# Performance work log

Measured on AMD Instinct MI355X. Metric: run time of the kernel, lower is better.

The kernel has to match this reference:

```python
import jax
import jax.numpy as jnp
import numpy as np

KSIZE, STRIDE, RATE, FUSE_K, SCALE = 3, 1, 2, 3, 10.0
ESCAPE_NAN = 1e-4


def _same_pad(x, k, s):
    # replicates torch same_padding: asymmetric zero pad so out = ceil(H/s)
    H, W = x.shape[2], x.shape[3]
    oh, ow = -(-H // s), -(-W // s)
    ph = max(0, (oh - 1) * s + k - H)
    pw = max(0, (ow - 1) * s + k - W)
    return jnp.pad(x, ((0, 0), (0, 0), (ph // 2, ph - ph // 2), (pw // 2, pw - pw // 2)))


def _extract_patches(x, k, s):
    # torch extract_image_patches: -> [B, L, C, k, k] with L = out_h*out_w
    x = _same_pad(x, k, s)
    B, C, H, W = x.shape
    Ho, Wo = (H - k) // s + 1, (W - k) // s + 1
    slices = [x[:, :, i:i + Ho * s:s, j:j + Wo * s:s] for i in range(k) for j in range(k)]
    p = jnp.stack(slices, axis=2).reshape(B, C, k, k, Ho, Wo)
    return p.transpose(0, 4, 5, 1, 2, 3).reshape(B, Ho * Wo, C, k, k)


def _contextual_attention(f, b, mask):
    dn = ('NCHW', 'OIHW', 'NCHW')
    # raw background patches for the final deconv: k = 2*rate, stride = rate
    raw_pat = _extract_patches(b, 2 * RATE, RATE * STRIDE)  # [B, L, C, 4, 4]
    # nearest-neighbor 1/rate downsample (torch F.interpolate nearest, sf=0.5)
    f_ds = f[:, :, ::RATE, ::RATE]
    b_ds = b[:, :, ::RATE, ::RATE]
    m_ds = mask[:, :, ::RATE, ::RATE]
    B, C, Hf, Wf = f_ds.shape
    Hb, Wb = b_ds.shape[2], b_ds.shape[3]
    b_pat = _extract_patches(b_ds, KSIZE, STRIDE)  # [B, L, C, 3, 3], L = Hb*Wb
    m_pat = _extract_patches(m_ds, KSIZE, STRIDE)[0]  # [L, 1, 3, 3] (first sample only, as in torch)
    mm = (jnp.mean(m_pat, axis=(1, 2, 3)) == 0.0).astype(f.dtype)[None, :, None, None]  # [1, L, 1, 1]
    fuse_w = jnp.eye(FUSE_K, dtype=f.dtype).reshape(1, 1, FUSE_K, FUSE_K)

    def per_item(xi, wi, raw_wi):
        # xi: [C,Hf,Wf]; wi: [L,C,3,3]; raw_wi: [L,C,4,4]
        max_wi = jnp.sqrt(jnp.sum(wi * wi + ESCAPE_NAN, axis=(1, 2, 3), keepdims=True))
        wi_n = wi / max_wi
        # matching conv: scores [1, L, Hf, Wf]
        yi = jax.lax.conv_general_dilated(xi[None], wi_n, (1, 1), ((1, 1), (1, 1)), dimension_numbers=dn)
        # fuse: identity-diagonal 3x3 conv along (bg_idx, fg_idx) twice with transposes
        yi = yi.reshape(1, 1, Hb * Wb, Hf * Wf)
        yi = jax.lax.conv_general_dilated(yi, fuse_w, (1, 1), ((1, 1), (1, 1)), dimension_numbers=dn)
        yi = yi.reshape(Hb, Wb, Hf, Wf).transpose(1, 0, 3, 2).reshape(1, 1, Hb * Wb, Hf * Wf)
        yi = jax.lax.conv_general_dilated(yi, fuse_w, (1, 1), ((1, 1), (1, 1)), dimension_numbers=dn)
        yi = yi.reshape(Wb, Hb, Wf, Hf).transpose(1, 0, 3, 2).reshape(1, Hb * Wb, Hf, Wf)
        yi = yi * mm
        yi = jax.nn.softmax(yi * SCALE, axis=1) * mm
        # conv_transpose2d(yi, raw_wi[I=L,O=C], stride=rate, padding=1) / 4
        w2 = jnp.flip(raw_wi, (2, 3)).transpose(1, 0, 2, 3)  # [C, L, 4, 4]
        pad = 2 * RATE - 1 - 1  # k - 1 - torch_padding = 2
        out = jax.lax.conv_general_dilated(yi, w2, (1, 1), ((pad, pad), (pad, pad)),
                                           lhs_dilation=(RATE, RATE), dimension_numbers=dn) / 4.0
        return out[0]

    return jax.vmap(per_item)(f_ds, b_pat, raw_pat)  # [B, C, H, W]


def setup_inputs() -> dict:
    key = jax.random.key(0)
    k1, k2 = jax.random.split(key)
    B, C, H, W = 2, 128, 128, 128
    f = jax.random.normal(k1, (B, C, H, W), dtype=jnp.float32)
    b = jax.random.normal(k2, (B, C, H, W), dtype=jnp.float32)
    mask = jnp.zeros((B, 1, H, W), dtype=jnp.float32)
    return {"f": f, "b": b, "mask": mask}


def reference(f, b, mask):
    return _contextual_attention(f, b, mask)
```

## Files before the change

### kernel.cpp

```cpp
#include <hip/hip_runtime.h>
#include <math.h>

#define CDIM 128
#define HF   128
#define WF   128
#define NP   4096
#define NCHUNK 64

typedef __attribute__((ext_vector_type(8))) short short8;
typedef __attribute__((ext_vector_type(16))) float f16a;
typedef float __attribute__((ext_vector_type(4), aligned(16))) f4a16;
typedef float __attribute__((ext_vector_type(4), aligned(4)))  f4u;

__device__ inline ushort f2bf(float x) {
  union { float f; unsigned u; } v; v.f = x;
  unsigned r = v.u + 0x7fff + ((v.u >> 16) & 1);
  return (ushort)(r >> 16);
}
__device__ inline float bf2f(ushort h) {
  union { unsigned u; float f; } v; v.u = ((unsigned)h) << 16; return v.f;
}

__device__ inline void gl2lds16(const ushort* g, ushort* l) {
  __builtin_amdgcn_global_load_lds((const __attribute__((address_space(1))) void*)g,
                                   (__attribute__((address_space(3))) void*)l, 16, 0, 0);
}

__global__ __launch_bounds__(256) void k_prep(const float* __restrict__ f,
                                              const float* __restrict__ b,
                                              ushort* __restrict__ fcat,
                                              ushort* __restrict__ bcat,
                                              float* __restrict__ s2) {
  int idx = blockIdx.x * 256 + threadIdx.x;
  int c = idx & 127, pos = idx >> 7;
  int x = pos & 63, y = pos >> 6;
  int src = c * 16384 + y * 256 + x * 2;
  float fv = f[src], bv = b[src];
  ushort fh = f2bf(fv); ushort fl = f2bf(fv - bf2f(fh));
  ushort bh = f2bf(bv); ushort bl = f2bf(bv - bf2f(bh));
  size_t base = (size_t)pos * 384;
  fcat[base + c] = fh; fcat[base + 128 + c] = fl; fcat[base + 256 + c] = fh;
  bcat[base + c] = bh; bcat[base + 128 + c] = bh; bcat[base + 256 + c] = bl;
  float sq = bv * bv;
#pragma unroll
  for (int off = 32; off; off >>= 1) sq += __shfl_down(sq, off);
  __shared__ float wsum[4];
  if ((threadIdx.x & 63) == 0) wsum[threadIdx.x >> 6] = sq;
  __syncthreads();
  if (threadIdx.x == 0) s2[blockIdx.x * 2]     = wsum[0] + wsum[1];
  if (threadIdx.x == 1) s2[blockIdx.x * 2 + 1] = wsum[2] + wsum[3];
}

__global__ __launch_bounds__(256) void k_mmpnorm(const float* __restrict__ mask,
                                                 const float* __restrict__ s2,
                                                 float* __restrict__ mmp,
                                                 float* __restrict__ rnrm) {
  int bx = blockIdx.x, t = threadIdx.x;
  if (bx < 16) {
    int a = bx * 256 + t;
    int yb = a & 63, xb = a >> 6;
    float s = 0.f;
    for (int dy = -1; dy <= 1; ++dy)
      for (int dx = -1; dx <= 1; ++dx) {
        int y = yb + dy, x = xb + dx;
        if ((unsigned)y < 64u && (unsigned)x < 64u)
          s += mask[y * 256 + x * 2];
      }
    mmp[a] = (s == 0.0f) ? 1.0f : 0.0f;
  } else {
    int p = (bx - 16) * 256 + t;
    int xb = p & 63, yb = p >> 6;
    float s = 0.f;
    for (int dy = -1; dy <= 1; ++dy)
      for (int dx = -1; dx <= 1; ++dx) {
        int y = yb + dy, x = xb + dx;
        if ((unsigned)y < 64u && (unsigned)x < 64u) s += s2[y * 64 + x];
      }
    rnrm[p] = rsqrtf(s + 1152.0f * 1.0e-4f);
  }
}

__global__ __launch_bounds__(512) void k_mfma_gemm(const ushort* __restrict__ A,
                                                   const ushort* __restrict__ B,
                                                   float* __restrict__ Out,
                                                   int Kdim, int lda, int ldb, int ldo,
                                                   long osplit) {
  __shared__ ushort As[2][256 * 64];
  __shared__ ushort Bs[2][256 * 64];
  const int tid = threadIdx.x;
  const int wave = tid >> 6, lane = tid & 63;
  const int l32 = lane & 31, khalf = lane >> 5;
  const int m0 = blockIdx.y * 256, n0 = blockIdx.x * 256;
  const int wm = (wave >> 2) * 128, wn = (wave & 3) * 64;
  const int srow = lane >> 3;
  const int gperm = ((lane & 7) ^ srow) * 8;

  const int koff = blockIdx.z * Kdim;
  A += koff; B += koff;
  Out += (size_t)blockIdx.z * osplit;

  const ushort* Ag = A + (size_t)(m0 + wave * 8 + srow) * lda + gperm;
  const ushort* Bg = B + (size_t)(n0 + wave * 8 + srow) * ldb + gperm;
  ushort* AsW = &As[0][0] + (wave * 8) * 64;
  ushort* BsW = &Bs[0][0] + (wave * 8) * 64;

#define STG_A(sl, tt, q) gl2lds16(Ag + (size_t)((q) * 64) * lda + ((tt) << 6), \
                                  AsW + (sl) * 16384 + (q) * 4096)
#define STG_B(sl, tt, q) gl2lds16(Bg + (size_t)((q) * 64) * ldb + ((tt) << 6), \
                                  BsW + (sl) * 16384 + (q) * 4096)

  f16a acc[4][2];
#pragma unroll
  for (int u = 0; u < 4; ++u)
#pragma unroll
    for (int v = 0; v < 2; ++v)
#pragma unroll
      for (int r = 0; r < 16; ++r) acc[u][v][r] = 0.f;

  const int NT = Kdim >> 6;

#pragma unroll
  for (int q = 0; q < 4; ++q) { STG_A(0, 0, q); STG_B(0, 0, q); }
  asm volatile("s_waitcnt vmcnt(0)" ::: "memory");
  __builtin_amdgcn_s_barrier();
  __builtin_amdgcn_sched_barrier(0);

  for (int t = 0; t < NT; ++t) {
    const int sl = t & 1;
    const ushort* Ar = &As[sl][0];
    const ushort* Br = &Bs[sl][0];
    short8 af[2][4], bf[2][2];

#define FRAG_READS(sidx) do { \
  _Pragma("unroll") for (int u = 0; u < 4; ++u) { \
    int am = wm + u * 32 + l32; \
    int ga = (((sidx) * 2 + khalf) ^ (am & 7)) * 8; \
    af[(sidx) & 1][u] = *reinterpret_cast<const short8*>(&Ar[am * 64 + ga]); } \
  _Pragma("unroll") for (int v = 0; v < 2; ++v) { \
    int bn = wn + v * 32 + l32; \
    int gb = (((sidx) * 2 + khalf) ^ (bn & 7)) * 8; \
    bf[(sidx) & 1][v] = *reinterpret_cast<const short8*>(&Br[bn * 64 + gb]); } \
} while (0)

    FRAG_READS(0);
    if (t + 1 < NT) {
#pragma unroll
      for (int q = 0; q < 4; ++q) STG_A(sl ^ 1, t + 1, q);
    }
    FRAG_READS(1);
    if (t + 1 < NT) {
#pragma unroll
      for (int q = 0; q < 4; ++q) STG_B(sl ^ 1, t + 1, q);
    }
#pragma unroll
    for (int s = 0; s < 4; ++s) {
      if (s == 1) FRAG_READS(2);
      if (s == 2) FRAG_READS(3);
      __builtin_amdgcn_s_setprio(1);
#pragma unroll
      for (int u = 0; u < 4; ++u)
#pragma unroll
        for (int v = 0; v < 2; ++v)
          acc[u][v] = __builtin_amdgcn_mfma_f32_32x32x16_bf16(af[s & 1][u], bf[s & 1][v],
                                                              acc[u][v], 0, 0, 0);
      __builtin_amdgcn_s_setprio(0);
    }
    if (t + 1 < NT) {
      asm volatile("s_waitcnt vmcnt(0)" ::: "memory");
      __builtin_amdgcn_s_barrier();
      __builtin_amdgcn_sched_barrier(0);
    }
#undef FRAG_READS
  }

#pragma unroll
  for (int u = 0; u < 4; ++u)
#pragma unroll
    for (int v = 0; v < 2; ++v)
#pragma unroll
      for (int r = 0; r < 16; ++r) {
        int row = (r & 3) + 8 * (r >> 2) + 4 * khalf;
        Out[(size_t)(m0 + wm + u * 32 + row) * ldo + (n0 + wn + v * 32 + l32)] = acc[u][v][r];
      }
#undef STG_A
#undef STG_B
}

__global__ __launch_bounds__(256) void k_s0(const float* __restrict__ D,
                                            const float* __restrict__ rnrm,
                                            float* __restrict__ S0) {
  int p = ((blockIdx.x & 7) << 9) | (blockIdx.x >> 3);
  int yb = p >> 6, xb = p & 63;
  float rp = rnrm[p];
  int t = threadIdx.x;
#pragma unroll
  for (int it = 0; it < 4; ++it) {
    int q = (it * 256 + t) << 2;
    int qy = q >> 6, qx = q & 63;
    f4a16 acc = (f4a16){0.f, 0.f, 0.f, 0.f};
#pragma unroll
    for (int dy = -1; dy <= 1; ++dy) {
      if ((unsigned)(yb + dy) >= 64u) continue;
      if ((unsigned)(qy + dy) >= 64u) continue;
#pragma unroll
      for (int dx = -1; dx <= 1; ++dx) {
        if ((unsigned)(xb + dx) >= 64u) continue;
        int delta = dy * 64 + dx;
        const float* base = D + (size_t)(p + delta) * 4096;
        f4u v;
        if (dx == -1 && qx == 0) {
          f4u r = *(const f4u*)(base + q + delta + 1);
          v = (f4u){0.f, r.x, r.y, r.z};
        } else {
          v = *(const f4u*)(base + q + delta);
          if (dx == 1 && qx == 60) v.w = 0.f;
        }
        acc += v;
      }
    }
    acc *= rp;
    *(f4a16*)(S0 + ((size_t)p << 12) + q) = acc;
  }
}

__global__ __launch_bounds__(256) void k_fuse1(const float* __restrict__ S0,
                                               float* __restrict__ Yp) {
  __shared__ float row[4160];
  int i = ((blockIdx.x & 7) << 9) | (blockIdx.x >> 3);
  int t = threadIdx.x;
  const float* r0 = S0 + (size_t)(i - 1) * 4096;
  const float* r1 = S0 + (size_t)i * 4096;
  const float* r2 = S0 + (size_t)(i + 1) * 4096;
  bool up = (i > 0), dn = (i < 4095);
#pragma unroll
  for (int jj = 0; jj < 4; ++jj) {
    int j = (jj * 256 + t) << 2;
    f4u s = *(const f4u*)(r1 + j);
    if (up) {
      f4u a;
      if (j == 0) { f4u r = *(const f4u*)r0; a = (f4u){0.f, r.x, r.y, r.z}; }
      else a = *(const f4u*)(r0 + j - 1);
      s += a;
    }
    if (dn) {
      f4u d = *(const f4u*)(r2 + j + 1);
      if (j == 4092) d.w = 0.f;
      s += d;
    }
    int base = j + (j >> 6);
    row[base + 0] = s.x; row[base + 1] = s.y; row[base + 2] = s.z; row[base + 3] = s.w;
  }
  __syncthreads();
  int a = ((i & 63) << 6) | (i >> 6);
  float* orow = Yp + ((size_t)a << 12);
#pragma unroll
  for (int bb = 0; bb < 4; ++bb) {
    int b4 = (bb * 256 + t) << 2;
    f4a16 o;
#pragma unroll
    for (int k = 0; k < 4; ++k) {
      int jT = (((b4 + k) & 63) << 6) | ((b4 + k) >> 6);
      o[k] = row[jT + (jT >> 6)];
    }
    *(f4a16*)(orow + b4) = o;
  }
}

__global__ __launch_bounds__(256) void k_smax_part(const float* __restrict__ Yp,
                                                   const float* __restrict__ mmp,
                                                   float* __restrict__ pm,
                                                   float* __restrict__ ps) {
  int v = (blockIdx.x * 256 + threadIdx.x) << 2;
  int chunk = blockIdx.y;
  f4a16 m = (f4a16){-1e30f, -1e30f, -1e30f, -1e30f};
  f4a16 s = (f4a16){0.f, 0.f, 0.f, 0.f};
  int u0 = chunk * (4096 / NCHUNK);
  for (int u = u0; u < u0 + (4096 / NCHUNK); ++u) {
    const float* row = Yp + ((size_t)u << 12);
    f4u tv = *(const f4u*)(row + v);
    if (u > 0) {
      f4u a;
      if (v == 0) { f4u r = *(const f4u*)(row - 4096); a = (f4u){0.f, r.x, r.y, r.z}; }
      else a = *(const f4u*)(row - 4096 + v - 1);
      tv += a;
    }
    if (u < 4095) {
      f4u d = *(const f4u*)(row + 4096 + v + 1);
      if (v == 4092) d.w = 0.f;
      tv += d;
    }
    float g = 10.0f * mmp[u];
    f4u x = tv * g;
#pragma unroll
    for (int l = 0; l < 4; ++l) {
      float xl = x[l];
      if (xl > m[l]) { s[l] = s[l] * __expf(m[l] - xl) + 1.0f; m[l] = xl; }
      else           { s[l] += __expf(xl - m[l]); }
    }
  }
  *(f4a16*)(pm + chunk * NP + v) = m;
  *(f4a16*)(ps + chunk * NP + v) = s;
}

__global__ __launch_bounds__(256) void k_epilogue(const float* __restrict__ Yp,
                                                  const float* __restrict__ pm,
                                                  const float* __restrict__ ps,
                                                  const float* __restrict__ mmp,
                                                  ushort* __restrict__ AT,
                                                  const float* __restrict__ bimg,
                                                  ushort* __restrict__ VtT) {
  __shared__ float T[64][65];
  __shared__ float pmS[4][64];
  __shared__ float psS[4][64];
  __shared__ float mS[64];
  __shared__ float rsS[64];
  int gx = blockIdx.x;
  int t = threadIdx.x;
  if (gx < 4096) {
    int a0 = (gx & 63) * 64, b0 = (gx >> 6) * 64;
    int j = t & 63, grp = t >> 6;
    float m = -1e30f, s = 0.f;
    for (int ch = grp * 16; ch < grp * 16 + 16; ++ch) {
      float m2 = pm[ch * NP + b0 + j], s2 = ps[ch * NP + b0 + j];
      if (m2 > m) { s = s * __expf(m - m2) + s2; m = m2; }
      else        { s += s2 * __expf(m2 - m); }
    }
    pmS[grp][j] = m; psS[grp][j] = s;
    __syncthreads();
    if (grp == 0) {
      for (int g2 = 1; g2 < 4; ++g2) {
        float m2 = pmS[g2][j], s2 = psS[g2][j];
        if (m2 > m) { s = s * __expf(m - m2) + s2; m = m2; }
        else        { s += s2 * __expf(m2 - m); }
      }
      mS[j] = m; rsS[j] = 1.0f / s;
    }
    __syncthreads();
    int i = t >> 4, j4 = (t & 15) << 2;
    f4a16 mc = *(const f4a16*)&mS[j4];
    f4a16 rs = *(const f4a16*)&rsS[j4];
#pragma unroll
    for (int r = 0; r < 4; ++r) {
      int al = r * 16 + i;
      int a = a0 + al;
      const float* row = Yp + ((size_t)a << 12);
      int b = b0 + j4;
      f4u y = *(const f4u*)(row + b);
      if (a > 0) {
        f4u u_;
        if (b == 0) { f4u rr = *(const f4u*)(row - 4096); u_ = (f4u){0.f, rr.x, rr.y, rr.z}; }
        else u_ = *(const f4u*)(row - 4096 + b - 1);
        y += u_;
      }
      if (a < 4095) {
        f4u d = *(const f4u*)(row + 4096 + b + 1);
        if (b == 4092) d.w = 0.f;
        y += d;
      }
      float g = mmp[a];
      f4u x = y * (10.0f * g);
#pragma unroll
      for (int l = 0; l < 4; ++l)
        T[al][j4 + l] = g * __expf(x[l] - mc[l]) * rs[l];
    }
    __syncthreads();
    int by0 = b0 >> 6;
    int cgrp = (t & 7) * 8;
#pragma unroll
    for (int pass = 0; pass < 2; ++pass) {
      int bl = pass * 32 + (t >> 3);
      int q = bl * 64 + by0;
      uint4 w;
      w.x = (unsigned)f2bf(T[cgrp + 0][bl]) | ((unsigned)f2bf(T[cgrp + 1][bl]) << 16);
      w.y = (unsigned)f2bf(T[cgrp + 2][bl]) | ((unsigned)f2bf(T[cgrp + 3][bl]) << 16);
      w.z = (unsigned)f2bf(T[cgrp + 4][bl]) | ((unsigned)f2bf(T[cgrp + 5][bl]) << 16);
      w.w = (unsigned)f2bf(T[cgrp + 6][bl]) | ((unsigned)f2bf(T[cgrp + 7][bl]) << 16);
      *(uint4*)(AT + ((size_t)q << 12) + a0 + cgrp) = w;
    }
  } else {
    int k2 = gx - 4096;
    int c = k2 >> 4, dy = (k2 >> 2) & 3, dx = k2 & 3;
    int px = t & 63;
#pragma unroll
    for (int r = 0; r < 16; ++r) {
      int py = r * 4 + (t >> 6);
      int sy = 2 * py + dy - 1, sx = 2 * px + dx - 1;
      float v = 0.f;
      if ((unsigned)sy < (unsigned)HF && (unsigned)sx < (unsigned)WF)
        v = bimg[c * 16384 + sy * 128 + sx];
      T[py][px] = v;
    }
    __syncthreads();
    ushort* orow = VtT + (size_t)k2 * 4096;
#pragma unroll
    for (int r = 0; r < 16; ++r) {
      int a = r * 256 + t;
      orow[a] = f2bf(T[a & 63][a >> 6]);
    }
  }
}

__global__ __launch_bounds__(256) void k_scatter(const float* __restrict__ Ma,
                                                 const float* __restrict__ Mb,
                                                 float* __restrict__ out) {
  int bid = ((blockIdx.x & 7) << 10) | (blockIdx.x >> 3);
  int idx = bid * 256 + threadIdx.x;
  int ox = idx & 127, oy = (idx >> 7) & 127, c = idx >> 14;
  int qy[2], dyv[2], qx[2], dxv[2];
  if (oy & 1) { qy[0] = (oy - 1) >> 1; dyv[0] = 2; qy[1] = (oy + 1) >> 1; dyv[1] = 0; }
  else        { qy[0] = (oy >> 1) - 1; dyv[0] = 3; qy[1] = oy >> 1;       dyv[1] = 1; }
  if (ox & 1) { qx[0] = (ox - 1) >> 1; dxv[0] = 2; qx[1] = (ox + 1) >> 1; dxv[1] = 0; }
  else        { qx[0] = (ox >> 1) - 1; dxv[0] = 3; qx[1] = ox >> 1;       dxv[1] = 1; }
  float s = 0.f;
#pragma unroll
  for (int i = 0; i < 2; ++i) {
    if ((unsigned)qy[i] >= 64u) continue;
#pragma unroll
    for (int j = 0; j < 2; ++j) {
      if ((unsigned)qx[j] >= 64u) continue;
      int k = c * 16 + dyv[i] * 4 + dxv[j];
      size_t off = (size_t)k * NP + qy[i] * 64 + qx[j];
      s += Ma[off] + Mb[off];
    }
  }
  out[idx] = 0.25f * s;
}

extern "C" void kernel_launch(void* const* d_in, const int* in_sizes, int n_in,
                              void* d_out, int out_size, void* d_ws, size_t ws_size,
                              hipStream_t stream) {
  const float* f_all = (const float*)d_in[0];
  const float* b_all = (const float*)d_in[1];
  const float* m_all = (const float*)d_in[2];
  float* out = (float*)d_out;

  float* ws = (float*)d_ws;
  float* bufD = ws;
  float* bufS = ws + 16777216;
  ushort* fcat = (ushort*)bufS;
  ushort* bcat = (ushort*)(bufS + 786432);
  float* S0  = bufS;
  float* Yp  = bufD;
  ushort* AT  = (ushort*)bufS;
  ushort* VtT = (ushort*)(bufS + 8388608);
  float* M0 = bufD;
  float* M1 = bufD + 8388608;
  float* smalls = ws + 2 * 16777216;
  float* s2    = smalls;
  float* rnrm  = s2 + 4096;
  float* mmp   = rnrm + 4096;
  float* pm    = mmp + 4096;
  float* ps    = pm + NCHUNK * NP;

  const size_t zsF = (size_t)CDIM * HF * WF;
  const size_t zsM = (size_t)HF * WF;

  for (int it = 0; it < 2; ++it) {
    const float* f = f_all + it * zsF;
    const float* b = b_all + it * zsF;
    const float* mk = m_all + it * zsM;
    float* o = out + it * zsF;

    k_prep<<<2048, 256, 0, stream>>>(f, b, fcat, bcat, s2);
    k_mmpnorm<<<32, 256, 0, stream>>>(mk, s2, mmp, rnrm);
    k_mfma_gemm<<<dim3(16, 16, 1), 512, 0, stream>>>(bcat, fcat, bufD, 384, 384, 384, NP, 0);
    k_s0<<<4096, 256, 0, stream>>>(bufD, rnrm, S0);
    k_fuse1<<<4096, 256, 0, stream>>>(S0, Yp);
    k_smax_part<<<dim3(4, NCHUNK), 256, 0, stream>>>(Yp, mmp, pm, ps);
    k_epilogue<<<6144, 256, 0, stream>>>(Yp, pm, ps, mmp, AT, b, VtT);
    k_mfma_gemm<<<dim3(16, 8, 2), 512, 0, stream>>>(VtT, AT, M0, 2048, NP, NP, NP,
                                                    (long)2048 * 4096);
    k_scatter<<<8192, 256, 0, stream>>>(M0, M1, o);
  }
}
```

Measured before the change: 610.1 us.

## Switch GEMM to 16x16x32 MFMA with phased barrier-synchronized LDS pipeline

Replaces the 32x32x16 bf16 MFMA tiles with 16x16x32 MFMA fragments (8x4 accumulators per wave) and restructures the K loop into a two-tile unrolled schedule. Each half-step issues LDS fragment reads and global-to-LDS prefetches, then runs a block-wide barrier before a priority-raised MFMA cluster, in a ping-pong-style phase schedule. The goal is better overlap of memory and matrix work and cheaper fragment reads. The cost is many more barriers per K tile and an unrolled loop that assumes NT is even.

```diff
diff --git a/kernel.cpp b/kernel.cpp
--- a/kernel.cpp
+++ b/kernel.cpp
@@ -8,7 +8,7 @@
 #define NCHUNK 64
 
 typedef __attribute__((ext_vector_type(8))) short short8;
-typedef __attribute__((ext_vector_type(16))) float f16a;
+typedef __attribute__((ext_vector_type(4))) float f32x4;
 typedef float __attribute__((ext_vector_type(4), aligned(16))) f4a16;
 typedef float __attribute__((ext_vector_type(4), aligned(4)))  f4u;
 
@@ -85,11 +85,11 @@
                                                    float* __restrict__ Out,
                                                    int Kdim, int lda, int ldb, int ldo,
                                                    long osplit) {
-  __shared__ ushort As[2][256 * 64];
-  __shared__ ushort Bs[2][256 * 64];
+  __shared__ ushort As[2][16384];
+  __shared__ ushort Bs[2][16384];
   const int tid = threadIdx.x;
   const int wave = tid >> 6, lane = tid & 63;
-  const int l32 = lane & 31, khalf = lane >> 5;
+  const int l16 = lane & 15, lgrp = lane >> 4;
   const int m0 = blockIdx.y * 256, n0 = blockIdx.x * 256;
   const int wm = (wave >> 2) * 128, wn = (wave & 3) * 64;
   const int srow = lane >> 3;
@@ -109,15 +109,46 @@
 #define STG_B(sl, tt, q) gl2lds16(Bg + (size_t)((q) * 64) * ldb + ((tt) << 6), \
                                   BsW + (sl) * 16384 + (q) * 4096)
 
-  f16a acc[4][2];
-#pragma unroll
-  for (int u = 0; u < 4; ++u)
-#pragma unroll
-    for (int v = 0; v < 2; ++v)
-#pragma unroll
-      for (int r = 0; r < 16; ++r) acc[u][v][r] = 0.f;
+#define DS_A(mh, ks_) do { \
+  _Pragma("unroll") for (int u = 0; u < 4; ++u) { \
+    int row = wm + ((mh) * 4 + u) * 16 + l16; \
+    int g = (((ks_) * 4 + lgrp) ^ (row & 7)) * 8; \
+    af[u] = *reinterpret_cast<const short8*>(&Ar[row * 64 + g]); } \
+} while (0)
+#define DS_B(ks_) do { \
+  _Pragma("unroll") for (int v = 0; v < 4; ++v) { \
+    int row = wn + v * 16 + l16; \
+    int g = (((ks_) * 4 + lgrp) ^ (row & 7)) * 8; \
+    bf[v] = *reinterpret_cast<const short8*>(&Br[row * 64 + g]); } \
+} while (0)
+#define MFMA16(mh) do { \
+  _Pragma("unroll") for (int u = 0; u < 4; ++u) \
+    _Pragma("unroll") for (int v = 0; v < 4; ++v) \
+      acc[(mh) * 4 + u][v] = __builtin_amdgcn_mfma_f32_16x16x32_bf16( \
+          af[u], bf[v], acc[(mh) * 4 + u][v], 0, 0, 0); \
+} while (0)
+#define PH_MID do { \
+  __builtin_amdgcn_sched_barrier(0); \
+  __builtin_amdgcn_s_barrier(); \
+  asm volatile("s_waitcnt lgkmcnt(0)" ::: "memory"); \
+  __builtin_amdgcn_sched_barrier(0); \
+  __builtin_amdgcn_s_setprio(1); \
+} while (0)
+#define PH_END do { \
+  __builtin_amdgcn_s_setprio(0); \
+  __builtin_amdgcn_s_barrier(); \
+  __builtin_amdgcn_sched_barrier(0); \
+} while (0)
+
+  f32x4 acc[8][4];
+#pragma unroll
+  for (int u = 0; u < 8; ++u)
+#pragma unroll
+    for (int v = 0; v < 4; ++v)
+      acc[u][v] = (f32x4){0.f, 0.f, 0.f, 0.f};
 
   const int NT = Kdim >> 6;
+  short8 af[4], bf[4];
 
 #pragma unroll
   for (int q = 0; q < 4; ++q) { STG_A(0, 0, q); STG_B(0, 0, q); }
@@ -125,65 +156,69 @@
   __builtin_amdgcn_s_barrier();
   __builtin_amdgcn_sched_barrier(0);
 
-  for (int t = 0; t < NT; ++t) {
-    const int sl = t & 1;
-    const ushort* Ar = &As[sl][0];
-    const ushort* Br = &Bs[sl][0];
-    short8 af[2][4], bf[2][2];
-
-#define FRAG_READS(sidx) do { \
-  _Pragma("unroll") for (int u = 0; u < 4; ++u) { \
-    int am = wm + u * 32 + l32; \
-    int ga = (((sidx) * 2 + khalf) ^ (am & 7)) * 8; \
-    af[(sidx) & 1][u] = *reinterpret_cast<const short8*>(&Ar[am * 64 + ga]); } \
-  _Pragma("unroll") for (int v = 0; v < 2; ++v) { \
-    int bn = wn + v * 32 + l32; \
-    int gb = (((sidx) * 2 + khalf) ^ (bn & 7)) * 8; \
-    bf[(sidx) & 1][v] = *reinterpret_cast<const short8*>(&Br[bn * 64 + gb]); } \
-} while (0)
-
-    FRAG_READS(0);
-    if (t + 1 < NT) {
-#pragma unroll
-      for (int q = 0; q < 4; ++q) STG_A(sl ^ 1, t + 1, q);
-    }
-    FRAG_READS(1);
-    if (t + 1 < NT) {
-#pragma unroll
-      for (int q = 0; q < 4; ++q) STG_B(sl ^ 1, t + 1, q);
-    }
-#pragma unroll
-    for (int s = 0; s < 4; ++s) {
-      if (s == 1) FRAG_READS(2);
-      if (s == 2) FRAG_READS(3);
-      __builtin_amdgcn_s_setprio(1);
-#pragma unroll
-      for (int u = 0; u < 4; ++u)
-#pragma unroll
-        for (int v = 0; v < 2; ++v)
-          acc[u][v] = __builtin_amdgcn_mfma_f32_32x32x16_bf16(af[s & 1][u], bf[s & 1][v],
-                                                              acc[u][v], 0, 0, 0);
+  for (int t0 = 0; t0 < NT; t0 += 2) {
+    const bool st = (t0 + 2) < NT;
+    {
+      const ushort* Ar = &As[0][0];
+      const ushort* Br = &Bs[0][0];
+      DS_B(0); DS_A(0, 0);
+#pragma unroll
+      for (int q = 0; q < 4; ++q) STG_A(1, t0 + 1, q);
+      PH_MID; MFMA16(0); PH_END;
+      DS_A(1, 0);
+#pragma unroll
+      for (int q = 0; q < 4; ++q) STG_B(1, t0 + 1, q);
+      PH_MID; MFMA16(1); PH_END;
+      DS_B(1); DS_A(0, 1);
+      PH_MID; MFMA16(0); PH_END;
+      DS_A(1, 1);
+      PH_MID; MFMA16(1);
       __builtin_amdgcn_s_setprio(0);
-    }
-    if (t + 1 < NT) {
       asm volatile("s_waitcnt vmcnt(0)" ::: "memory");
       __builtin_amdgcn_s_barrier();
       __builtin_amdgcn_sched_barrier(0);
     }
-#undef FRAG_READS
-  }
-
-#pragma unroll
-  for (int u = 0; u < 4; ++u)
-#pragma unroll
-    for (int v = 0; v < 2; ++v)
-#pragma unroll
-      for (int r = 0; r < 16; ++r) {
-        int row = (r & 3) + 8 * (r >> 2) + 4 * khalf;
-        Out[(size_t)(m0 + wm + u * 32 + row) * ldo + (n0 + wn + v * 32 + l32)] = acc[u][v][r];
-      }
+    {
+      const ushort* Ar = &As[1][0];
+      const ushort* Br = &Bs[1][0];
+      DS_B(0); DS_A(0, 0);
+      if (st) {
+#pragma unroll
+        for (int q = 0; q < 4; ++q) STG_A(0, t0 + 2, q);
+      }
+      PH_MID; MFMA16(0); PH_END;
+      DS_A(1, 0);
+      if (st) {
+#pragma unroll
+        for (int q = 0; q < 4; ++q) STG_B(0, t0 + 2, q);
+      }
+      PH_MID; MFMA16(1); PH_END;
+      DS_B(1); DS_A(0, 1);
+      PH_MID; MFMA16(0); PH_END;
+      DS_A(1, 1);
+      PH_MID; MFMA16(1);
+      __builtin_amdgcn_s_setprio(0);
+      if (st) asm volatile("s_waitcnt vmcnt(0)" ::: "memory");
+      __builtin_amdgcn_s_barrier();
+      __builtin_amdgcn_sched_barrier(0);
+    }
+  }
+
+#pragma unroll
+  for (int mf = 0; mf < 8; ++mf)
+#pragma unroll
+    for (int nf = 0; nf < 4; ++nf)
+#pragma unroll
+      for (int r = 0; r < 4; ++r)
+        Out[(size_t)(m0 + wm + mf * 16 + lgrp * 4 + r) * ldo + (n0 + wn + nf * 16 + l16)] =
+            acc[mf][nf][r];
 #undef STG_A
 #undef STG_B
+#undef DS_A
+#undef DS_B
+#undef MFMA16
+#undef PH_MID
+#undef PH_END
 }
 
 __global__ __launch_bounds__(256) void k_s0(const float* __restrict__ D,
```

Result: no change. 619.3 us (+1.5%).
